# Kernel tuning notes

Measured on AMD Instinct MI355X. Metric: run time of the kernel, lower is better.

## Reference

```python
import jax, jax.numpy as jnp
import numpy as np

B, NM, T, RED = 8, 10, 16376, 8
D, H, L = 512, 8, 4
DH = D // H
BS, NG, NW, NR = 64, 1, 3, 2
S = T // RED + 1          # 2048 tokens incl. CLS
NB = S // BS              # 32 blocks
FF = 2048


def _ln(x, g, b):
    m = x.mean(-1, keepdims=True)
    v = ((x - m) ** 2).mean(-1, keepdims=True)
    return (x - m) / jnp.sqrt(v + 1e-5) * g + b


def setup_inputs() -> dict:
    key = jax.random.key(0)
    ks = jax.random.split(key, 16)
    p = lambda k, sh: jax.random.normal(k, sh, jnp.float32) * 0.02
    return {
        "x": jax.random.normal(ks[0], (B, NM, T), jnp.float32),
        "w_embed": p(ks[1], (NM * RED, D)), "b_embed": jnp.zeros((D,), jnp.float32),
        "pos_emb": p(ks[2], (S, D)),
        "Wq": p(ks[3], (L, D, D)), "bq": jnp.zeros((L, D), jnp.float32),
        "Wk": p(ks[4], (L, D, D)), "bk": jnp.zeros((L, D), jnp.float32),
        "Wv": p(ks[5], (L, D, D)), "bv": jnp.zeros((L, D), jnp.float32),
        "Wo": p(ks[6], (L, D, D)), "bo": jnp.zeros((L, D), jnp.float32),
        "ln1_g": jnp.ones((L, D), jnp.float32), "ln1_b": jnp.zeros((L, D), jnp.float32),
        "W1": p(ks[7], (L, D, FF)), "b1": jnp.zeros((L, FF), jnp.float32),
        "W2": p(ks[8], (L, FF, D)), "b2": jnp.zeros((L, D), jnp.float32),
        "ln2_g": jnp.ones((L, D), jnp.float32), "ln2_b": jnp.zeros((L, D), jnp.float32),
        "w_dense": p(ks[9], (D, 1024)), "b_dense": jnp.zeros((1024,), jnp.float32),
        "w_out": p(ks[10], (1024, 2)), "b_out": jnp.zeros((2,), jnp.float32),
        "rand_blocks": jax.random.randint(ks[11], (NB, NR), 0, NB),
    }


def _fwd(x, w_embed, b_embed, pos_emb, Wq, bq, Wk, bk, Wv, bv, Wo, bo,
         ln1_g, ln1_b, W1, b1, W2, b2, ln2_g, ln2_b,
         w_dense, b_dense, w_out, b_out, rand_blocks):
    Bx = x.shape[0]
    # [B, NM, T] -> view [B, NM*RED, T//RED] -> transpose -> [B, S-1, NM*RED]
    h = x.reshape(Bx, NM * RED, -1).transpose(0, 2, 1)
    h = h @ w_embed + b_embed
    cls = jnp.zeros((Bx, 1, D), h.dtype)
    h = jnp.concatenate([cls, h], axis=1) + pos_emb[None]  # learned pos-enc

    # block-sparse context: static global + window blocks, dynamic random blocks
    win = np.clip(np.arange(NB)[:, None] + np.arange(NW)[None, :] - NW // 2, 0, NB - 1)
    glb = np.broadcast_to(np.arange(NG)[None, :], (NB, NG))
    idx = jnp.concatenate([jnp.asarray(np.concatenate([glb, win], 1)), rand_blocks], axis=1)  # [NB, C]
    C = idx.shape[1]
    # mask context blocks that duplicate an earlier block for the same query block
    dup = jnp.tril(idx[:, :, None] == idx[:, None, :], -1).any(-1)  # [NB, C]
    scale = 1.0 / np.sqrt(DH)

    for l in range(L):
        def heads(w, b):
            return (h @ w + b).reshape(Bx, S, H, DH).transpose(0, 2, 1, 3).reshape(Bx, H, NB, BS, DH)
        q, k, v = heads(Wq[l], bq[l]), heads(Wk[l], bk[l]), heads(Wv[l], bv[l])
        kg, vg = k[:, :, idx], v[:, :, idx]             # [B, H, NB, C, BS, DH] block gather
        sc = jnp.einsum('bhnqd,bhncsd->bhnqcs', q, kg) * scale
        sc = jnp.where(dup[None, None, :, None, :, None], -1e9, sc)
        attn = jax.nn.softmax(sc.reshape(Bx, H, NB, BS, C * BS), axis=-1).reshape(sc.shape)
        o = jnp.einsum('bhnqcs,bhncsd->bhnqd', attn, vg)
        o = o.reshape(Bx, H, S, DH).transpose(0, 2, 1, 3).reshape(Bx, S, D) @ Wo[l] + bo[l]
        h = _ln(h + o, ln1_g[l], ln1_b[l])
        ff = jax.nn.relu(h @ W1[l] + b1[l]) @ W2[l] + b2[l]
        h = _ln(h + ff, ln2_g[l], ln2_b[l])

    dense = jax.nn.relu(h[:, 0] @ w_dense + b_dense)  # CLS readout
    return jnp.tanh(dense @ w_out + b_out)            # [B, 2]


def reference(x, w_embed, b_embed, pos_emb, Wq, bq, Wk, bk, Wv, bv, Wo, bo,
              ln1_g, ln1_b, W1, b1, W2, b2, ln2_g, ln2_b,
              w_dense, b_dense, w_out, b_out, rand_blocks):
    return _fwd(x, w_embed, b_embed, pos_emb, Wq, bq, Wk, bk, Wv, bv, Wo, bo,
                ln1_g, ln1_b, W1, b1, W2, b2, ln2_g, ln2_b,
                w_dense, b_dense, w_out, b_out, rand_blocks)
```

## Files before the change

### kernel.cpp

```cpp
#include <hip/hip_runtime.h>
#include <cstdint>
#include <cstddef>

#define B_   8
#define NM_  10
#define T_   16376
#define D_   512
#define H_   8
#define DH_  64
#define L_   4
#define S_   2048
#define NB_  32
#define BS_  64
#define FF_  2048
#define MTOK (B_*S_)
#define DD_  (D_*D_)
#define KE_  128

typedef __attribute__((ext_vector_type(8))) __bf16 bf16x8;
typedef __attribute__((ext_vector_type(4))) __bf16 bf16x4;
typedef __attribute__((ext_vector_type(4))) float f32x4;

__device__ __forceinline__ void async16(void* lds, const void* g) {
    __builtin_amdgcn_global_load_lds(
        (const __attribute__((address_space(1))) void*)g,
        (__attribute__((address_space(3))) void*)lds, 16, 0, 0);
}

#define SWZ64(row, kq) (((row) << 3) + ((kq) ^ ((row) & 7)))

__global__ __launch_bounds__(256) void wconv_kernel(
    const float* __restrict__ in, __bf16* __restrict__ outp, int K, int N, int Kp)
{
    __shared__ float t[32][33];
    const float* ip = in + (size_t)blockIdx.z * K * N;
    __bf16* op = outp + (size_t)blockIdx.z * N * Kp;
    int n0 = blockIdx.x * 32, k0 = blockIdx.y * 32;
    int tx = threadIdx.x, ty = threadIdx.y;
    #pragma unroll
    for (int j = 0; j < 4; j++) {
        int k = k0 + ty + 8 * j;
        t[ty + 8 * j][tx] = (k < K) ? ip[(size_t)k * N + n0 + tx] : 0.f;
    }
    __syncthreads();
    #pragma unroll
    for (int j = 0; j < 4; j++)
        op[(size_t)(n0 + ty + 8 * j) * Kp + k0 + tx] = (__bf16)t[tx][ty + 8 * j];
}

__global__ __launch_bounds__(256) void wconv_qkvo(
    const float* __restrict__ wq, const float* __restrict__ wk,
    const float* __restrict__ wv, const float* __restrict__ wo,
    __bf16* __restrict__ wtqkv, __bf16* __restrict__ wto)
{
    __shared__ float t[32][33];
    int zz = blockIdx.z;
    int mat = zz >> 2, layer = zz & 3;
    const float* src = (mat == 0 ? wq : mat == 1 ? wk : mat == 2 ? wv : wo)
                       + (size_t)layer * DD_;
    __bf16* dst = (mat < 3) ? wtqkv + ((size_t)mat * L_ + layer) * DD_
                            : wto + (size_t)layer * DD_;
    int n0 = blockIdx.x * 32, k0 = blockIdx.y * 32;
    int tx = threadIdx.x, ty = threadIdx.y;
    #pragma unroll
    for (int j = 0; j < 4; j++)
        t[ty + 8 * j][tx] = src[(size_t)(k0 + ty + 8 * j) * D_ + n0 + tx];
    __syncthreads();
    #pragma unroll
    for (int j = 0; j < 4; j++)
        dst[(size_t)(n0 + ty + 8 * j) * D_ + k0 + tx] = (__bf16)t[tx][ty + 8 * j];
}

__global__ __launch_bounds__(256) void xbuild_kernel(
    const float* __restrict__ x, __bf16* __restrict__ xr)
{
    __shared__ float xs[64][KE_ + 1];
    int row0 = blockIdx.x * 64;
    int b = row0 >> 11;
    int t0 = row0 & (S_ - 1);
    int tid = threadIdx.x;
    int lane = tid & 63;
    int mq = tid >> 6;
    for (int mb = 0; mb < 32; mb++) {
        int m = mb * 4 + mq;
        int t = t0 + lane;
        float v = 0.f;
        if (m < 80 && t > 0)
            v = x[(size_t)b * NM_ * T_ + (size_t)(m >> 3) * T_ + (m & 7) * 2047 + (t - 1)];
        xs[lane][m] = v;
    }
    __syncthreads();
    #pragma unroll
    for (int u = 0; u < 8; u++) {
        int ch = tid + u * 256;
        int row = ch >> 5, c4 = (ch & 31) * 4;
        bf16x4 pk;
        #pragma unroll
        for (int i = 0; i < 4; i++) pk[i] = (__bf16)xs[row][c4 + i];
        *(bf16x4*)&xr[(size_t)(row0 + row) * KE_ + c4] = pk;
    }
}

__global__ __launch_bounds__(512, 2) void mfma_gemm(
    const __bf16* __restrict__ A, const __bf16* __restrict__ Wt,
    const float* __restrict__ bias0, const float* __restrict__ bias1,
    const float* __restrict__ bias2,
    const float* __restrict__ pe, float* __restrict__ Cf, __bf16* __restrict__ Cb,
    int N, int K, long wtz, long cbz, int relu, int scatter, int nz)
{
    __shared__ __align__(16) __bf16 As[3 * 256 * 64];
    __shared__ __align__(16) __bf16 Bs[3 * 128 * 64];
    int tid = threadIdx.x;
    int wave = tid >> 6;
    int lane = tid & 63;

    int nbx = gridDim.x, nby = gridDim.y;
    int bxIdx, bmIdx;
    if ((nby & 7) == 0) {
        int id = blockIdx.y * nbx + blockIdx.x;
        int chunk = nby >> 3;
        int xcd = id & 7;
        int local = id >> 3;
        int row = local / nbx;
        bmIdx = xcd * chunk + row;
        bxIdx = local - row * nbx;
    } else {
        bxIdx = blockIdx.x; bmIdx = blockIdx.y;
    }
    int z = bxIdx % nz;
    int bn = (bxIdx / nz) * 128;
    int bm = bmIdx * 256;
    const __bf16* Wz = Wt + (size_t)z * wtz;
    const float* bias = (z == 0) ? bias0 : (z == 1 ? bias1 : bias2);

    f32x4 acc[4][4];
    #pragma unroll
    for (int r = 0; r < 4; r++)
        #pragma unroll
        for (int c = 0; c < 4; c++) acc[r][c] = (f32x4){0.f, 0.f, 0.f, 0.f};

    const int wr = (wave >> 1) * 64;
    const int wc = (wave & 1) * 64;
    const int fr = lane & 15;
    const int kqi = lane >> 4;

    const __bf16* pA[4];
    const __bf16* pB[2];
    int ldsA[4], ldsB[2];
    #pragma unroll
    for (int u = 0; u < 4; u++) {
        int p = tid + 512 * u;
        int row = p >> 3;
        int kq = (p & 7) ^ (row & 7);
        pA[u] = A + (size_t)(bm + row) * K + kq * 8;
        ldsA[u] = (u * 512 + wave * 64) * 8;
    }
    #pragma unroll
    for (int u = 0; u < 2; u++) {
        int p = tid + 512 * u;
        int row = p >> 3;
        int kq = (p & 7) ^ (row & 7);
        pB[u] = Wz + (size_t)(bn + row) * K + kq * 8;
        ldsB[u] = (u * 512 + wave * 64) * 8;
    }

    __bf16 *a0 = As, *a1 = As + 256 * 64, *a2 = As + 2 * 256 * 64;
    __bf16 *b0 = Bs, *b1 = Bs + 128 * 64, *b2 = Bs + 2 * 128 * 64;

    #pragma unroll
    for (int u = 0; u < 4; u++) async16(a0 + ldsA[u], pA[u]);
    #pragma unroll
    for (int u = 0; u < 2; u++) async16(b0 + ldsB[u], pB[u]);
    asm volatile("" ::: "memory");
    #pragma unroll
    for (int u = 0; u < 4; u++) async16(a1 + ldsA[u], pA[u] + 64);
    #pragma unroll
    for (int u = 0; u < 2; u++) async16(b1 + ldsB[u], pB[u] + 64);
    asm volatile("s_waitcnt vmcnt(6)\n\ts_barrier" ::: "memory");

    const int NT = K >> 6;
    for (int t = 0; t < NT; ++t) {
        if (t + 2 < NT) {
            int kk = (t + 2) * 64;
            #pragma unroll
            for (int u = 0; u < 4; u++) async16(a2 + ldsA[u], pA[u] + kk);
            #pragma unroll
            for (int u = 0; u < 2; u++) async16(b2 + ldsB[u], pB[u] + kk);
        }
        #pragma unroll
        for (int ks = 0; ks < 2; ks++) {
            int kq0 = ks * 4 + kqi;
            bf16x8 af[4], bfr[4];
            #pragma unroll
            for (int r = 0; r < 4; r++)
                af[r] = *(const bf16x8*)&a0[SWZ64(wr + r * 16 + fr, kq0) * 8];
            #pragma unroll
            for (int c = 0; c < 4; c++)
                bfr[c] = *(const bf16x8*)&b0[SWZ64(wc + c * 16 + fr, kq0) * 8];
            __builtin_amdgcn_s_setprio(1);
            #pragma unroll
            for (int r = 0; r < 4; r++)
                #pragma unroll
                for (int c = 0; c < 4; c++)
                    acc[r][c] = __builtin_amdgcn_mfma_f32_16x16x32_bf16(af[r], bfr[c], acc[r][c], 0, 0, 0);
            __builtin_amdgcn_s_setprio(0);
        }
        if (t + 2 < NT) asm volatile("s_waitcnt vmcnt(6)\n\ts_barrier" ::: "memory");
        else            asm volatile("s_waitcnt vmcnt(0)\n\ts_barrier" ::: "memory");
        __bf16* ta = a0; a0 = a1; a1 = a2; a2 = ta;
        __bf16* tb = b0; b0 = b1; b1 = b2; b2 = tb;
    }

    int rbase = bm + wr + (lane >> 4) * 4;
    #pragma unroll
    for (int c = 0; c < 4; c++) {
        int cg = bn + wc + c * 16 + fr;
        float bv = bias[cg];
        #pragma unroll
        for (int r = 0; r < 4; r++) {
            int rg0 = rbase + r * 16;
            float vals[4];
            #pragma unroll
            for (int i = 0; i < 4; i++) {
                float val = acc[r][c][i] + bv;
                if (relu) val = fmaxf(val, 0.f);
                if (pe) {
                    int t = (rg0 + i) & (S_ - 1);
                    val = (t == 0) ? pe[cg] : val + pe[(size_t)t * N + cg];
                }
                vals[i] = val;
            }
            if (Cf) {
                #pragma unroll
                for (int i = 0; i < 4; i++) Cf[(size_t)(rg0 + i) * N + cg] = vals[i];
            }
            if (Cb) {
                if (scatter) {
                    int bb = rg0 >> 11;
                    int s0 = rg0 & (S_ - 1);
                    int hh = cg >> 6, dh = cg & 63;
                    if (z == 2) {
                        bf16x4 pk;
                        #pragma unroll
                        for (int i = 0; i < 4; i++) pk[i] = (__bf16)vals[i];
                        *(bf16x4*)(Cb + (size_t)z * cbz +
                                   ((((size_t)bb * H_ + hh) * DH_ + dh) * S_) + s0) = pk;
                    } else {
                        #pragma unroll
                        for (int i = 0; i < 4; i++)
                            (Cb + (size_t)z * cbz)[((((size_t)bb * H_ + hh) * S_ + s0 + i) * DH_) + dh] = (__bf16)vals[i];
                    }
                } else {
                    #pragma unroll
                    for (int i = 0; i < 4; i++) Cb[(size_t)(rg0 + i) * N + cg] = (__bf16)vals[i];
                }
            }
        }
    }
}

#define KSTR 72
__global__ __launch_bounds__(256, 4) void attn_kernel(
    const __bf16* __restrict__ q, const __bf16* __restrict__ k,
    const __bf16* __restrict__ vt, const int* __restrict__ rb,
    __bf16* __restrict__ o)
{
    __shared__ __align__(16) __bf16 Ks[64 * KSTR];
    __shared__ __align__(16) __bf16 Vs[64 * KSTR];
    __shared__ __align__(16) __bf16 Ps[64 * KSTR];
    int bid = blockIdx.x;
    int xcd = bid & 7;
    int local = bid >> 3;
    int bh = (local >> 5) * 8 + xcd;
    int n = local & 31;
    int b = bh >> 3;
    int hh = bh & 7;
    int tid = threadIdx.x;
    int wave = tid >> 6;
    int lane = tid & 63;
    const int fr = lane & 15;
    const int fq = lane >> 4;

    int idx[6];
    idx[0] = 0;
    idx[1] = n > 0 ? n - 1 : 0;
    idx[2] = n;
    idx[3] = n < NB_ - 1 ? n + 1 : NB_ - 1;
    idx[4] = rb[n * 2 + 0];
    idx[5] = rb[n * 2 + 1];

    const size_t plane = ((size_t)b * H_ + hh) * S_;
    const __bf16* vtb = vt + plane * DH_;

    const __bf16* qrow = q + (plane + (size_t)n * BS_ + wave * 16 + fr) * DH_ + fq * 8;
    bf16x8 qf0 = *(const bf16x8*)qrow;
    bf16x8 qf1 = *(const bf16x8*)(qrow + 32);

    f32x4 oacc[4];
    #pragma unroll
    for (int dt = 0; dt < 4; dt++) oacc[dt] = (f32x4){0.f, 0.f, 0.f, 0.f};
    float mrow = -1e30f, lrow = 0.f;

    for (int c = 0; c < 6; c++) {
        bool dup = false;
        #pragma unroll
        for (int j = 0; j < 6; j++) if (j < c && idx[j] == idx[c]) dup = true;
        if (dup) continue;

        __syncthreads();
        {
            const __bf16* kb = k + (plane + (size_t)idx[c] * BS_) * DH_;
            const __bf16* vb = vtb + (size_t)idx[c] * BS_;
            #pragma unroll
            for (int u = 0; u < 2; u++) {
                int ch = tid + u * 256;
                int row = ch >> 3, d0 = (ch & 7) * 8;
                *(bf16x8*)&Ks[row * KSTR + d0] = *(const bf16x8*)(kb + row * DH_ + d0);
                *(bf16x8*)&Vs[row * KSTR + d0] = *(const bf16x8*)(vb + (size_t)row * S_ + d0);
            }
        }
        __syncthreads();

        f32x4 st[4];
        #pragma unroll
        for (int t = 0; t < 4; t++) {
            bf16x8 ka0 = *(const bf16x8*)&Ks[(t * 16 + fr) * KSTR + fq * 8];
            bf16x8 ka1 = *(const bf16x8*)&Ks[(t * 16 + fr) * KSTR + 32 + fq * 8];
            st[t] = __builtin_amdgcn_mfma_f32_16x16x32_bf16(ka0, qf0, (f32x4){0.f,0.f,0.f,0.f}, 0, 0, 0);
            st[t] = __builtin_amdgcn_mfma_f32_16x16x32_bf16(ka1, qf1, st[t], 0, 0, 0);
        }
        float rmax = -1e30f;
        #pragma unroll
        for (int t = 0; t < 4; t++)
            #pragma unroll
            for (int i = 0; i < 4; i++) {
                st[t][i] *= 0.125f;
                rmax = fmaxf(rmax, st[t][i]);
            }
        rmax = fmaxf(rmax, __shfl_xor(rmax, 16));
        rmax = fmaxf(rmax, __shfl_xor(rmax, 32));
        float newm = fmaxf(mrow, rmax);
        float corr = __expf(mrow - newm);
        mrow = newm;
        float psum = 0.f;
        #pragma unroll
        for (int t = 0; t < 4; t++) {
            bf16x4 pk;
            #pragma unroll
            for (int i = 0; i < 4; i++) {
                float p = __expf(st[t][i] - newm);
                psum += p;
                pk[i] = (__bf16)p;
            }
            *(bf16x4*)&Ps[(wave * 16 + fr) * KSTR + t * 16 + fq * 4] = pk;
        }
        psum += __shfl_xor(psum, 16);
        psum += __shfl_xor(psum, 32);
        lrow = lrow * corr + psum;

        #pragma unroll
        for (int i = 0; i < 4; i++) {
            float ci = __shfl(corr, fq * 4 + i);
            #pragma unroll
            for (int dt = 0; dt < 4; dt++) oacc[dt][i] *= ci;
        }

        bf16x8 pa0 = *(const bf16x8*)&Ps[(wave * 16 + fr) * KSTR + fq * 8];
        bf16x8 pa1 = *(const bf16x8*)&Ps[(wave * 16 + fr) * KSTR + 32 + fq * 8];
        #pragma unroll
        for (int dt = 0; dt < 4; dt++) {
            bf16x8 vb0 = *(const bf16x8*)&Vs[(dt * 16 + fr) * KSTR + fq * 8];
            bf16x8 vb1 = *(const bf16x8*)&Vs[(dt * 16 + fr) * KSTR + 32 + fq * 8];
            oacc[dt] = __builtin_amdgcn_mfma_f32_16x16x32_bf16(pa0, vb0, oacc[dt], 0, 0, 0);
            oacc[dt] = __builtin_amdgcn_mfma_f32_16x16x32_bf16(pa1, vb1, oacc[dt], 0, 0, 0);
        }
    }

    float linv = 1.f / lrow;
    #pragma unroll
    for (int i = 0; i < 4; i++) {
        float li = __shfl(linv, fq * 4 + i);
        int s = n * BS_ + wave * 16 + fq * 4 + i;
        __bf16* op = o + ((size_t)b * S_ + s) * D_ + hh * DH_ + fr;
        #pragma unroll
        for (int dt = 0; dt < 4; dt++)
            op[dt * 16] = (__bf16)(oacc[dt][i] * li);
    }
}

__global__ __launch_bounds__(256) void ln_add_kernel(
    float* h, const __bf16* __restrict__ delta, __bf16* __restrict__ hb,
    const float* __restrict__ g, const float* __restrict__ bb)
{
    size_t r = (size_t)blockIdx.x * 4 + (threadIdx.x >> 6);
    int t = threadIdx.x & 63;
    float4* hp = (float4*)(h + r * D_) + 2 * t;
    float4 x0 = hp[0], x1 = hp[1];
    bf16x8 dv = *(const bf16x8*)&delta[r * D_ + t * 8];
    float x[8] = {x0.x, x0.y, x0.z, x0.w, x1.x, x1.y, x1.z, x1.w};
    #pragma unroll
    for (int j = 0; j < 8; j++) x[j] += (float)dv[j];
    float s = 0.f;
    #pragma unroll
    for (int j = 0; j < 8; j++) s += x[j];
    #pragma unroll
    for (int off = 32; off; off >>= 1) s += __shfl_xor(s, off, 64);
    float mean = s * (1.0f / D_);
    float ss = 0.f;
    #pragma unroll
    for (int j = 0; j < 8; j++) { x[j] -= mean; ss += x[j] * x[j]; }
    #pragma unroll
    for (int off = 32; off; off >>= 1) ss += __shfl_xor(ss, off, 64);
    float rs = rsqrtf(ss * (1.0f / D_) + 1e-5f);
    float4 g0 = ((const float4*)g)[2 * t], g1 = ((const float4*)g)[2 * t + 1];
    float4 b0 = ((const float4*)bb)[2 * t], b1 = ((const float4*)bb)[2 * t + 1];
    float gg[8] = {g0.x, g0.y, g0.z, g0.w, g1.x, g1.y, g1.z, g1.w};
    float bbv[8] = {b0.x, b0.y, b0.z, b0.w, b1.x, b1.y, b1.z, b1.w};
    float y[8];
    bf16x8 outv;
    #pragma unroll
    for (int j = 0; j < 8; j++) {
        y[j] = x[j] * rs * gg[j] + bbv[j];
        outv[j] = (__bf16)y[j];
    }
    hp[0] = (float4){y[0], y[1], y[2], y[3]};
    hp[1] = (float4){y[4], y[5], y[6], y[7]};
    *(bf16x8*)&hb[r * D_ + t * 8] = outv;
}

__global__ __launch_bounds__(256) void head1_kernel(
    const float* __restrict__ h, const float* __restrict__ wd,
    const float* __restrict__ bd, const float* __restrict__ wo,
    float* __restrict__ partial)
{
    __shared__ float hrow[D_];
    __shared__ float red[8];
    int b = blockIdx.x, jg = blockIdx.y;
    int tid = threadIdx.x;
    if (tid < 128) ((float4*)hrow)[tid] = ((const float4*)(h + (size_t)b * S_ * D_))[tid];
    __syncthreads();
    int j = jg * 256 + tid;
    float acc = bd[j];
    #pragma unroll 8
    for (int i = 0; i < D_; i++) acc = fmaf(hrow[i], wd[(size_t)i * 1024 + j], acc);
    float dns = fmaxf(acc, 0.f);
    float2 w2 = ((const float2*)wo)[j];
    float p0 = dns * w2.x, p1 = dns * w2.y;
    #pragma unroll
    for (int off = 32; off; off >>= 1) { p0 += __shfl_xor(p0, off, 64); p1 += __shfl_xor(p1, off, 64); }
    int wid = tid >> 6;
    if ((tid & 63) == 0) { red[wid * 2] = p0; red[wid * 2 + 1] = p1; }
    __syncthreads();
    if (tid == 0) {
        float t0 = red[0] + red[2] + red[4] + red[6];
        float t1 = red[1] + red[3] + red[5] + red[7];
        partial[((size_t)b * 4 + jg) * 2 + 0] = t0;
        partial[((size_t)b * 4 + jg) * 2 + 1] = t1;
    }
}

__global__ __launch_bounds__(64) void head2_kernel(
    const float* __restrict__ partial, const float* __restrict__ bo,
    float* __restrict__ out)
{
    int tid = threadIdx.x;
    if (tid < 16) {
        int b = tid >> 1, c = tid & 1;
        float s = bo[c];
        #pragma unroll
        for (int jg = 0; jg < 4; jg++) s += partial[((size_t)b * 4 + jg) * 2 + c];
        out[b * 2 + c] = tanhf(s);
    }
}

extern "C" void kernel_launch(void* const* d_in, const int* in_sizes, int n_in,
                              void* d_out, int out_size, void* d_ws, size_t ws_size,
                              hipStream_t stream) {
    (void)in_sizes; (void)n_in; (void)out_size; (void)ws_size;
    const float* x       = (const float*)d_in[0];
    const float* w_embed = (const float*)d_in[1];
    const float* b_embed = (const float*)d_in[2];
    const float* pos_emb = (const float*)d_in[3];
    const float* Wq      = (const float*)d_in[4];
    const float* bq      = (const float*)d_in[5];
    const float* Wk      = (const float*)d_in[6];
    const float* bk      = (const float*)d_in[7];
    const float* Wv      = (const float*)d_in[8];
    const float* bv      = (const float*)d_in[9];
    const float* Wo      = (const float*)d_in[10];
    const float* bo      = (const float*)d_in[11];
    const float* ln1_g   = (const float*)d_in[12];
    const float* ln1_b   = (const float*)d_in[13];
    const float* W1      = (const float*)d_in[14];
    const float* b1      = (const float*)d_in[15];
    const float* W2      = (const float*)d_in[16];
    const float* b2      = (const float*)d_in[17];
    const float* ln2_g   = (const float*)d_in[18];
    const float* ln2_b   = (const float*)d_in[19];
    const float* w_dense = (const float*)d_in[20];
    const float* b_dense = (const float*)d_in[21];
    const float* w_out   = (const float*)d_in[22];
    const float* b_out   = (const float*)d_in[23];
    const int*   rb      = (const int*)d_in[24];
    float* out = (float*)d_out;

    const size_t PLANE = (size_t)B_ * H_ * S_ * DH_;
    float*  h    = (float*)d_ws;
    __bf16* h_bf = (__bf16*)((char*)d_ws + (size_t)32 * 1024 * 1024);
    __bf16* big  = (__bf16*)((char*)d_ws + (size_t)48 * 1024 * 1024);
    __bf16* qkv  = big;
    __bf16* o_bf = big + 3 * PLANE;
    __bf16* ff1  = big;
    __bf16* xr   = big;
    __bf16* wt_e = big + (size_t)28 * 1024 * 1024;
    __bf16* wt   = (__bf16*)((char*)d_ws + (size_t)112 * 1024 * 1024);
    __bf16* wt_qkv = wt;
    __bf16* wt_o   = wt_qkv + (size_t)3 * L_ * DD_;
    __bf16* wt_1   = wt_o + (size_t)L_ * DD_;
    __bf16* wt_2   = wt_1 + (size_t)L_ * D_ * FF_;
    __bf16* dbuf   = (__bf16*)((char*)d_ws + (size_t)138 * 1024 * 1024);
    float*  hpart  = (float*)((char*)d_ws + (size_t)154 * 1024 * 1024);

    dim3 tb(32, 8);
    wconv_qkvo<<<dim3(16, 16, 16), tb, 0, stream>>>(Wq, Wk, Wv, Wo, wt_qkv, wt_o);
    wconv_kernel<<<dim3(64, 16, L_), tb, 0, stream>>>(W1, wt_1, D_, FF_, D_);
    wconv_kernel<<<dim3(16, 64, L_), tb, 0, stream>>>(W2, wt_2, FF_, D_, FF_);
    wconv_kernel<<<dim3(16, 4, 1),  tb, 0, stream>>>(w_embed, wt_e, 80, D_, KE_);

    xbuild_kernel<<<MTOK / 64, 256, 0, stream>>>(x, xr);
    mfma_gemm<<<dim3(D_ / 128, MTOK / 256, 1), 512, 0, stream>>>(
        xr, wt_e, b_embed, b_embed, b_embed,
        pos_emb, h, h_bf, D_, KE_, 0, 0, 0, 0, 1);

    for (int l = 0; l < L_; l++) {
        mfma_gemm<<<dim3((D_ / 128) * 3, MTOK / 256, 1), 512, 0, stream>>>(
            h_bf, wt_qkv + (size_t)l * DD_, bq + l * D_, bk + l * D_, bv + l * D_,
            nullptr, nullptr, qkv, D_, D_, (long)L_ * DD_, (long)PLANE, 0, 1, 3);

        attn_kernel<<<B_ * H_ * NB_, 256, 0, stream>>>(qkv, qkv + PLANE, qkv + 2 * PLANE, rb, o_bf);

        mfma_gemm<<<dim3(D_ / 128, MTOK / 256, 1), 512, 0, stream>>>(
            o_bf, wt_o + (size_t)l * DD_, bo + l * D_, bo + l * D_, bo + l * D_,
            nullptr, nullptr, dbuf, D_, D_, 0, 0, 0, 0, 1);
        ln_add_kernel<<<MTOK / 4, 256, 0, stream>>>(h, dbuf, h_bf, ln1_g + l * D_, ln1_b + l * D_);

        mfma_gemm<<<dim3(FF_ / 128, MTOK / 256, 1), 512, 0, stream>>>(
            h_bf, wt_1 + (size_t)l * D_ * FF_, b1 + l * FF_, b1 + l * FF_, b1 + l * FF_,
            nullptr, nullptr, ff1, FF_, D_, 0, 0, 1, 0, 1);

        mfma_gemm<<<dim3(D_ / 128, MTOK / 256, 1), 512, 0, stream>>>(
            ff1, wt_2 + (size_t)l * FF_ * D_, b2 + l * D_, b2 + l * D_, b2 + l * D_,
            nullptr, nullptr, dbuf, D_, FF_, 0, 0, 0, 0, 1);
        ln_add_kernel<<<MTOK / 4, 256, 0, stream>>>(h, dbuf, h_bf, ln2_g + l * D_, ln2_b + l * D_);
    }

    head1_kernel<<<dim3(B_, 4), 256, 0, stream>>>(h, w_dense, b_dense, w_out, hpart);
    head2_kernel<<<1, 64, 0, stream>>>(hpart, b_out, out);
}
```

Before: 1.217 ms.

## Interleave async tile prefetch with split-K MFMA phases in GEMM main loop

Restructures the triple-buffered GEMM main loop into two half-K phases. Each phase issues half of the next tile's async global-to-LDS loads between its fragment reads and its MFMA block, with extra barriers around the MFMA blocks. Buffers are indexed by a rotating counter instead of swapped pointers. The aim is to spread memory issue across the compute and keep waves in lockstep so loads overlap better with matrix math. The cost is four barriers per iteration instead of one, and the vmcnt accounting is more delicate.

```diff
diff --git a/kernel.cpp b/kernel.cpp
--- a/kernel.cpp
+++ b/kernel.cpp
@@ -108,8 +108,8 @@
     const float* __restrict__ pe, float* __restrict__ Cf, __bf16* __restrict__ Cb,
     int N, int K, long wtz, long cbz, int relu, int scatter, int nz)
 {
-    __shared__ __align__(16) __bf16 As[3 * 256 * 64];
-    __shared__ __align__(16) __bf16 Bs[3 * 128 * 64];
+    __shared__ __align__(16) __bf16 As[3][256 * 64];
+    __shared__ __align__(16) __bf16 Bs[3][128 * 64];
     int tid = threadIdx.x;
     int wave = tid >> 6;
     int lane = tid & 63;
@@ -145,8 +145,7 @@
     const int kqi = lane >> 4;
 
     const __bf16* pA[4];
-    const __bf16* pB[2];
-    int ldsA[4], ldsB[2];
+    int ldsA[4];
     #pragma unroll
     for (int u = 0; u < 4; u++) {
         int p = tid + 512 * u;
@@ -155,6 +154,8 @@
         pA[u] = A + (size_t)(bm + row) * K + kq * 8;
         ldsA[u] = (u * 512 + wave * 64) * 8;
     }
+    const __bf16* pB[2];
+    int ldsB[2];
     #pragma unroll
     for (int u = 0; u < 2; u++) {
         int p = tid + 512 * u;
@@ -164,39 +165,43 @@
         ldsB[u] = (u * 512 + wave * 64) * 8;
     }
 
-    __bf16 *a0 = As, *a1 = As + 256 * 64, *a2 = As + 2 * 256 * 64;
-    __bf16 *b0 = Bs, *b1 = Bs + 128 * 64, *b2 = Bs + 2 * 128 * 64;
-
-    #pragma unroll
-    for (int u = 0; u < 4; u++) async16(a0 + ldsA[u], pA[u]);
-    #pragma unroll
-    for (int u = 0; u < 2; u++) async16(b0 + ldsB[u], pB[u]);
+    #pragma unroll
+    for (int u = 0; u < 4; u++) async16(As[0] + ldsA[u], pA[u]);
+    #pragma unroll
+    for (int u = 0; u < 2; u++) async16(Bs[0] + ldsB[u], pB[u]);
     asm volatile("" ::: "memory");
     #pragma unroll
-    for (int u = 0; u < 4; u++) async16(a1 + ldsA[u], pA[u] + 64);
-    #pragma unroll
-    for (int u = 0; u < 2; u++) async16(b1 + ldsB[u], pB[u] + 64);
-    asm volatile("s_waitcnt vmcnt(6)\n\ts_barrier" ::: "memory");
+    for (int u = 0; u < 4; u++) async16(As[1] + ldsA[u], pA[u] + 64);
+    #pragma unroll
+    for (int u = 0; u < 2; u++) async16(Bs[1] + ldsB[u], pB[u] + 64);
+    asm volatile("s_waitcnt vmcnt(6)" ::: "memory");
+    __builtin_amdgcn_s_barrier();
 
     const int NT = K >> 6;
+    int cur = 0;
     for (int t = 0; t < NT; ++t) {
-        if (t + 2 < NT) {
-            int kk = (t + 2) * 64;
-            #pragma unroll
-            for (int u = 0; u < 4; u++) async16(a2 + ldsA[u], pA[u] + kk);
-            #pragma unroll
-            for (int u = 0; u < 2; u++) async16(b2 + ldsB[u], pB[u] + kk);
-        }
-        #pragma unroll
-        for (int ks = 0; ks < 2; ks++) {
-            int kq0 = ks * 4 + kqi;
+        const __bf16* a_c = As[cur];
+        const __bf16* b_c = Bs[cur];
+        int n2 = cur + 2; if (n2 >= 3) n2 -= 3;
+        __bf16* a_n = As[n2];
+        __bf16* b_n = Bs[n2];
+        const int kk2 = (t + 2) * 64;
+        const bool pf = (t + 2 < NT);
+
+        {
             bf16x8 af[4], bfr[4];
             #pragma unroll
             for (int r = 0; r < 4; r++)
-                af[r] = *(const bf16x8*)&a0[SWZ64(wr + r * 16 + fr, kq0) * 8];
+                af[r] = *(const bf16x8*)&a_c[SWZ64(wr + r * 16 + fr, kqi) * 8];
             #pragma unroll
             for (int c = 0; c < 4; c++)
-                bfr[c] = *(const bf16x8*)&b0[SWZ64(wc + c * 16 + fr, kq0) * 8];
+                bfr[c] = *(const bf16x8*)&b_c[SWZ64(wc + c * 16 + fr, kqi) * 8];
+            if (pf) {
+                async16(a_n + ldsA[0], pA[0] + kk2);
+                async16(a_n + ldsA[1], pA[1] + kk2);
+                async16(a_n + ldsA[2], pA[2] + kk2);
+            }
+            __builtin_amdgcn_s_barrier();
             __builtin_amdgcn_s_setprio(1);
             #pragma unroll
             for (int r = 0; r < 4; r++)
@@ -204,11 +209,34 @@
                 for (int c = 0; c < 4; c++)
                     acc[r][c] = __builtin_amdgcn_mfma_f32_16x16x32_bf16(af[r], bfr[c], acc[r][c], 0, 0, 0);
             __builtin_amdgcn_s_setprio(0);
-        }
-        if (t + 2 < NT) asm volatile("s_waitcnt vmcnt(6)\n\ts_barrier" ::: "memory");
-        else            asm volatile("s_waitcnt vmcnt(0)\n\ts_barrier" ::: "memory");
-        __bf16* ta = a0; a0 = a1; a1 = a2; a2 = ta;
-        __bf16* tb = b0; b0 = b1; b1 = b2; b2 = tb;
+            __builtin_amdgcn_s_barrier();
+        }
+        {
+            bf16x8 af[4], bfr[4];
+            #pragma unroll
+            for (int r = 0; r < 4; r++)
+                af[r] = *(const bf16x8*)&a_c[SWZ64(wr + r * 16 + fr, 4 + kqi) * 8];
+            #pragma unroll
+            for (int c = 0; c < 4; c++)
+                bfr[c] = *(const bf16x8*)&b_c[SWZ64(wc + c * 16 + fr, 4 + kqi) * 8];
+            if (pf) {
+                async16(a_n + ldsA[3], pA[3] + kk2);
+                async16(b_n + ldsB[0], pB[0] + kk2);
+                async16(b_n + ldsB[1], pB[1] + kk2);
+            }
+            __builtin_amdgcn_s_barrier();
+            __builtin_amdgcn_s_setprio(1);
+            #pragma unroll
+            for (int r = 0; r < 4; r++)
+                #pragma unroll
+                for (int c = 0; c < 4; c++)
+                    acc[r][c] = __builtin_amdgcn_mfma_f32_16x16x32_bf16(af[r], bfr[c], acc[r][c], 0, 0, 0);
+            __builtin_amdgcn_s_setprio(0);
+            if (pf)                 asm volatile("s_waitcnt vmcnt(6)" ::: "memory");
+            else if (t + 1 < NT)    asm volatile("s_waitcnt vmcnt(0)" ::: "memory");
+            __builtin_amdgcn_s_barrier();
+        }
+        cur = cur + 1; if (cur == 3) cur = 0;
     }
 
     int rbase = bm + wr + (lane >> 4) * 4;
```

Measured after the change: 1.186 ms. 1.03x faster.
